# Performance work log

Measured on AMD Instinct MI355X. Metric: run time of the kernel, lower is better.

Reference implementation:

```python
import jax, jax.numpy as jnp
import numpy as np

E = 262144   # number of edges
B = 8192     # buckets per grouping
D = 32       # uniform bucket degree (B*D == E)
DIM = 128    # in_feats
OUT = 128    # out_feats


def setup_inputs() -> dict:
    key = jax.random.key(0)
    ks = jax.random.split(key, 12)
    src_feat = jax.random.normal(ks[0], (E, DIM), jnp.float32)
    dst_feat = jax.random.normal(ks[1], (E, DIM), jnp.float32)
    timestamp = jax.random.uniform(ks[2], (E,), jnp.float32) * 100.0
    # grouping permutations: flat edge order -> buckets of uniform degree
    src_perm = jax.random.permutation(ks[3], E).astype(jnp.int32)
    dst_perm = jax.random.permutation(ks[4], E).astype(jnp.int32)
    # causal deg_indices: index of most recent valid temporal neighbor, <= position
    pos = jnp.arange(D, dtype=jnp.int32)[None, :]
    src_deg_indices = jnp.minimum(jax.random.randint(ks[5], (B, D), 0, D, jnp.int32), pos)
    dst_deg_indices = jnp.minimum(jax.random.randint(ks[6], (B, D), 0, D, jnp.int32), pos)
    # TimeEncodingLayer('cosine') params
    basis_freq = 0.1 * jnp.linspace(0.0, 9.0, DIM, dtype=jnp.float32)
    phase = jnp.zeros((DIM,), jnp.float32)
    W_time = jax.random.normal(ks[7], (DIM, 2 * DIM), jnp.float32) * 0.05
    b_time = jnp.zeros((DIM,), jnp.float32)
    # fc_self / fc_neigh
    W_self = jax.random.normal(ks[8], (OUT, DIM), jnp.float32) * 0.05
    b_self = jnp.zeros((OUT,), jnp.float32)
    W_neigh = jax.random.normal(ks[9], (OUT, DIM), jnp.float32) * 0.05
    b_neigh = jnp.zeros((OUT,), jnp.float32)
    return dict(src_feat=src_feat, dst_feat=dst_feat, timestamp=timestamp,
                basis_freq=basis_freq, phase=phase, W_time=W_time, b_time=b_time,
                W_self=W_self, b_self=b_self, W_neigh=W_neigh, b_neigh=b_neigh,
                src_perm=src_perm, dst_perm=dst_perm,
                src_deg_indices=src_deg_indices, dst_deg_indices=dst_deg_indices)


def _encode_time(u, t, basis_freq, phase, W_time, b_time):
    # cosine time encoding: cos(t * freq + phase), concat with u, linear, relu
    tt = jnp.cos(t[:, None] * basis_freq[None, :] + phase[None, :])  # [E, DIM]
    x = jnp.concatenate([u, tt], axis=-1) @ W_time.T + b_time
    return jax.nn.relu(x)


def _mean_conv(h_self_e, h_neigh_e, perm, idx, W_self, b_self, W_neigh, b_neigh):
    # gather flat edge features into [B, D, DIM] buckets
    hs = h_self_e[perm].reshape(B, D, DIM)
    hn = h_neigh_e[perm].reshape(B, D, DIM)
    # mean aggregator: cumsum / (deg_indices+1), then gather at deg_indices
    mean_cof = (idx.astype(hn.dtype) + 1.0)[:, :, None]          # [B, D, 1]
    h_feat = jnp.cumsum(hn, axis=1) / mean_cof                    # [B, D, DIM]
    mask_feat = jnp.take_along_axis(h_feat, idx[:, :, None], axis=1)  # [B, D, DIM]
    rst = hs @ W_self.T + b_self + mask_feat @ W_neigh.T + b_neigh    # [B, D, OUT]
    # scatter back to flat edge order
    return jnp.zeros((E, OUT), rst.dtype).at[perm].set(rst.reshape(E, OUT))


def reference(src_feat, dst_feat, timestamp, basis_freq, phase, W_time, b_time,
              W_self, b_self, W_neigh, b_neigh,
              src_perm, dst_perm, src_deg_indices, dst_deg_indices):
    enc_src = _encode_time(src_feat, timestamp, basis_freq, phase, W_time, b_time)
    enc_dst = _encode_time(dst_feat, timestamp, basis_freq, phase, W_time, b_time)
    # groupby='src': self = src embedding, neighbors = dst embeddings
    src_out = _mean_conv(enc_src, enc_dst, src_perm, src_deg_indices,
                         W_self, b_self, W_neigh, b_neigh)
    # groupby='dst': self = dst embedding, neighbors = src embeddings
    dst_out = _mean_conv(enc_dst, enc_src, dst_perm, dst_deg_indices,
                         W_self, b_self, W_neigh, b_neigh)
    return src_out, dst_out
```

## Files before the change

kernel.cpp:

```cpp
#include <hip/hip_runtime.h>
#include <hip/hip_bf16.h>
#include <math.h>

#define E_EDGES 262144
#define NBUCKET 8192
#define DEG     32
#define FDIM    128

typedef float f32x4 __attribute__((ext_vector_type(4)));
typedef short s16x8 __attribute__((ext_vector_type(8)));
typedef short s16x4 __attribute__((ext_vector_type(4)));

typedef const __attribute__((address_space(1))) unsigned g_u32;
typedef __attribute__((address_space(3))) unsigned l_u32;

__device__ __forceinline__ short f2bf(float f) {
    __hip_bfloat16 h = __float2bfloat16(f);
    return *reinterpret_cast<short*>(&h);
}
__device__ __forceinline__ float bf2f(short s) {
    union { unsigned u; float f; } v; v.u = ((unsigned)(unsigned short)s) << 16;
    return v.f;
}

__device__ __forceinline__ s16x8 read_wfrag(const short* w_lds, int n, int k0) {
    int byte = ((n << 8) + (k0 << 1)) ^ ((n & 7) << 4);
    return *reinterpret_cast<const s16x8*>(reinterpret_cast<const char*>(w_lds) + byte);
}

__device__ __forceinline__ void stage_w(short* w_lds, const float* __restrict__ Wg,
                                        int stride, int tid) {
    #pragma unroll
    for (int it = 0; it < 16; ++it) {
        int i  = it * 256 + tid;
        int n  = i >> 5;
        int k4 = (i & 31) << 2;
        const float4 v = *reinterpret_cast<const float4*>(Wg + (size_t)n * stride + k4);
        s16x4 h; h[0]=f2bf(v.x); h[1]=f2bf(v.y); h[2]=f2bf(v.z); h[3]=f2bf(v.w);
        int byte = ((n << 8) + (k4 << 1)) ^ ((n & 7) << 4);
        *reinterpret_cast<s16x4*>(reinterpret_cast<char*>(w_lds) + byte) = h;
    }
}

__device__ __forceinline__ void dma_w32k(const short* __restrict__ gsw, short* lds, int tid) {
    const int lane = tid & 63, wid = tid >> 6;
    const char* g = reinterpret_cast<const char*>(gsw);
    char* l = reinterpret_cast<char*>(lds);
    #pragma unroll
    for (int i = 0; i < 8; ++i) {
        const int off = i * 4096 + wid * 1024;
        __builtin_amdgcn_global_load_lds((g_u32*)(g + off + lane * 16),
                                         (l_u32*)(l + off), 16, 0, 0);
    }
}

__global__ void prep_kernel(const float* __restrict__ W_time,
                            const float* __restrict__ W_self,
                            const float* __restrict__ W_neigh,
                            short* __restrict__ Wswz)
{
    const int t = blockIdx.x * 256 + threadIdx.x;
    const int region = t >> 11;
    const int chunk  = t & 2047;
    const int n = chunk >> 4;
    const int c = chunk & 15;

    const float* src;
    if      (region == 0) src = W_time  + n * 256 + c * 8;
    else if (region == 1) src = W_time  + n * 256 + 128 + c * 8;
    else if (region == 2) src = W_self  + n * 128 + c * 8;
    else                  src = W_neigh + n * 128 + c * 8;

    const float4 lo = *reinterpret_cast<const float4*>(src);
    const float4 hi = *reinterpret_cast<const float4*>(src + 4);
    s16x8 h;
    h[0]=f2bf(lo.x); h[1]=f2bf(lo.y); h[2]=f2bf(lo.z); h[3]=f2bf(lo.w);
    h[4]=f2bf(hi.x); h[5]=f2bf(hi.y); h[6]=f2bf(hi.z); h[7]=f2bf(hi.w);

    const int byte = (region << 15) + ((((n << 8) + (c << 4)) ^ ((n & 7) << 4)));
    *reinterpret_cast<s16x8*>(reinterpret_cast<char*>(Wswz) + byte) = h;
}

__global__ __launch_bounds__(512, 4)
void encode_kernel(const float* __restrict__ src_feat,
                   const float* __restrict__ dst_feat,
                   const float* __restrict__ ts,
                   const float* __restrict__ freq,
                   const float* __restrict__ ph,
                   const short* __restrict__ Wswz,
                   const float* __restrict__ b_time,
                   short* __restrict__ enc_src,
                   short* __restrict__ enc_dst)
{
    __shared__ short w_lds[2][128 * 128];

    const int tid  = threadIdx.x;
    const int lane = tid & 63;
    const int wid  = tid >> 6;
    const int lrow = lane & 15;
    const int q    = lane >> 4;
    const int klo  = q << 3;
    const int r0   = blockIdx.x * 128 + wid * 16;

    float4 sf[8], df[8];
    #pragma unroll
    for (int kb = 0; kb < 4; ++kb) {
        const float* ps = src_feat + (size_t)(r0 + lrow) * FDIM + kb * 32 + klo;
        const float* pd = dst_feat + (size_t)(r0 + lrow) * FDIM + kb * 32 + klo;
        sf[kb*2]   = *reinterpret_cast<const float4*>(ps);
        sf[kb*2+1] = *reinterpret_cast<const float4*>(ps + 4);
        df[kb*2]   = *reinterpret_cast<const float4*>(pd);
        df[kb*2+1] = *reinterpret_cast<const float4*>(pd + 4);
    }

    {
        const char* g = reinterpret_cast<const char*>(Wswz);
        char* l = reinterpret_cast<char*>(&w_lds[0][0]);
        #pragma unroll
        for (int i = 0; i < 8; ++i) {
            const int off = i * 8192 + wid * 1024;
            __builtin_amdgcn_global_load_lds((g_u32*)(g + off + lane * 16),
                                             (l_u32*)(l + off), 16, 0, 0);
        }
    }

    const float t_row = ts[r0 + lrow];
    s16x8 tf[4];
    #pragma unroll
    for (int kb = 0; kb < 4; ++kb) {
        s16x8 t;
        #pragma unroll
        for (int j = 0; j < 8; ++j) {
            const int k = kb * 32 + klo + j;
            t[j] = f2bf(__cosf(fmaf(t_row, freq[k], ph[k])));
        }
        tf[kb] = t;
    }

    s16x8 as_[4], ad_[4];
    #pragma unroll
    for (int kb = 0; kb < 4; ++kb) {
        s16x8 a, b;
        #pragma unroll
        for (int j = 0; j < 4; ++j) {
            a[j]   = f2bf(sf[kb*2][j]);   a[4+j] = f2bf(sf[kb*2+1][j]);
            b[j]   = f2bf(df[kb*2][j]);   b[4+j] = f2bf(df[kb*2+1][j]);
        }
        as_[kb] = a; ad_[kb] = b;
    }
    __syncthreads();

    #pragma unroll
    for (int nt = 0; nt < 8; ++nt) {
        const int n = nt * 16 + lrow;
        f32x4 a = {0.f, 0.f, 0.f, 0.f};
        #pragma unroll
        for (int kb = 0; kb < 4; ++kb)
            a = __builtin_amdgcn_mfma_f32_16x16x32_bf16(
                    read_wfrag(w_lds[1], n, kb * 32 + klo), tf[kb], a, 0, 0, 0);
        f32x4 b = a;
        #pragma unroll
        for (int kb = 0; kb < 4; ++kb) {
            const s16x8 wf = read_wfrag(w_lds[0], n, kb * 32 + klo);
            a = __builtin_amdgcn_mfma_f32_16x16x32_bf16(wf, as_[kb], a, 0, 0, 0);
            b = __builtin_amdgcn_mfma_f32_16x16x32_bf16(wf, ad_[kb], b, 0, 0, 0);
        }
        const int ch = nt * 16 + q * 4;
        const float4 bias4 = *reinterpret_cast<const float4*>(b_time + ch);
        s16x4 ss, sd;
        #pragma unroll
        for (int r = 0; r < 4; ++r) {
            float es = a[r] + bias4[r]; es = es > 0.f ? es : 0.f;
            float ed = b[r] + bias4[r]; ed = ed > 0.f ? ed : 0.f;
            ss[r] = f2bf(es); sd[r] = f2bf(ed);
        }
        *reinterpret_cast<s16x4*>(enc_src + (size_t)(r0 + lrow) * FDIM + ch) = ss;
        *reinterpret_cast<s16x4*>(enc_dst + (size_t)(r0 + lrow) * FDIM + ch) = sd;
    }
}

__global__ __launch_bounds__(256, 2)
void encode_fallback(const float* __restrict__ src_feat,
                     const float* __restrict__ dst_feat,
                     const float* __restrict__ ts,
                     const float* __restrict__ freq,
                     const float* __restrict__ ph,
                     const float* __restrict__ W_time,
                     const float* __restrict__ b_time,
                     short* __restrict__ enc_src,
                     short* __restrict__ enc_dst)
{
    __shared__ short w_lds[128 * 128];
    const int tid  = threadIdx.x;
    const int lane = tid & 63;
    const int wid  = tid >> 6;
    const int r0   = blockIdx.x * 64 + wid * 16;
    const int lrow = lane & 15;
    const int klo  = (lane >> 4) << 3;

    stage_w(w_lds, W_time + 128, 256, tid);
    const float t_row = ts[r0 + lrow];
    s16x8 tf[4];
    #pragma unroll
    for (int kb = 0; kb < 4; ++kb) {
        const int k = kb * 32 + klo;
        s16x8 t;
        #pragma unroll
        for (int j = 0; j < 8; ++j)
            t[j] = f2bf(__cosf(fmaf(t_row, freq[k + j], ph[k + j])));
        tf[kb] = t;
    }
    __syncthreads();
    f32x4 S[8];
    #pragma unroll
    for (int nt = 0; nt < 8; ++nt) {
        f32x4 a = {0.f, 0.f, 0.f, 0.f};
        #pragma unroll
        for (int kb = 0; kb < 4; ++kb)
            a = __builtin_amdgcn_mfma_f32_16x16x32_bf16(
                    tf[kb], read_wfrag(w_lds, nt * 16 + lrow, kb * 32 + klo), a, 0, 0, 0);
        S[nt] = a;
    }
    __syncthreads();
    stage_w(w_lds, W_time, 256, tid);
    __syncthreads();
    #pragma unroll
    for (int s = 0; s < 2; ++s) {
        const float* feat = s ? dst_feat : src_feat;
        short*       enc  = s ? enc_dst  : enc_src;
        s16x8 af[4];
        #pragma unroll
        for (int kb = 0; kb < 4; ++kb) {
            const float* p = feat + (size_t)(r0 + lrow) * FDIM + kb * 32 + klo;
            const float4 lo = *reinterpret_cast<const float4*>(p);
            const float4 hi = *reinterpret_cast<const float4*>(p + 4);
            s16x8 a;
            a[0]=f2bf(lo.x); a[1]=f2bf(lo.y); a[2]=f2bf(lo.z); a[3]=f2bf(lo.w);
            a[4]=f2bf(hi.x); a[5]=f2bf(hi.y); a[6]=f2bf(hi.z); a[7]=f2bf(hi.w);
            af[kb] = a;
        }
        #pragma unroll
        for (int nt = 0; nt < 8; ++nt) {
            f32x4 acc = S[nt];
            #pragma unroll
            for (int kb = 0; kb < 4; ++kb)
                acc = __builtin_amdgcn_mfma_f32_16x16x32_bf16(
                        af[kb], read_wfrag(w_lds, nt * 16 + lrow, kb * 32 + klo), acc, 0, 0, 0);
            const int col  = nt * 16 + lrow;
            const float bias = b_time[col];
            const int rbase = r0 + ((lane >> 4) << 2);
            #pragma unroll
            for (int r = 0; r < 4; ++r) {
                float e = acc[r] + bias;
                e = e > 0.f ? e : 0.f;
                enc[(size_t)(rbase + r) * FDIM + col] = f2bf(e);
            }
        }
    }
}

template<int DMA>
__global__ __launch_bounds__(256, 3)
void conv_kernel(const short* __restrict__ enc_src,
                 const short* __restrict__ enc_dst,
                 const short* __restrict__ Wswz_self,
                 const short* __restrict__ Wswz_neigh,
                 const float* __restrict__ W_self,
                 const float* __restrict__ W_neigh,
                 const float* __restrict__ b_self,
                 const float* __restrict__ b_neigh,
                 const int* __restrict__ src_perm,
                 const int* __restrict__ dst_perm,
                 const int* __restrict__ src_idx,
                 const int* __restrict__ dst_idx,
                 float* __restrict__ out)
{
    __shared__ short w_lds[128 * 128];
    __shared__ short hf[2][DEG * 128];
    __shared__ int   perm_s[2][DEG];
    __shared__ int   idx_s[2][DEG];
    __shared__ float bias_s[128];

    const int tid = threadIdx.x;
    const int g   = blockIdx.y;
    const int b0  = blockIdx.x * 2;

    const short* enc_self  = g ? enc_dst : enc_src;
    const short* enc_neigh = g ? enc_src : enc_dst;
    const int*   perm      = g ? dst_perm : src_perm;
    const int*   degi      = g ? dst_idx  : src_idx;
    float*       outg      = out + (size_t)g * E_EDGES * FDIM;

    if (DMA) dma_w32k(Wswz_self, w_lds, tid);

    if (tid < 64) {
        const int lb = tid >> 5, d = tid & 31;
        perm_s[lb][d] = perm[(b0 + lb) * DEG + d];
        idx_s[lb][d]  = degi[(b0 + lb) * DEG + d];
    } else if (tid < 192) {
        const int c = tid - 64;
        bias_s[c] = b_self[c] + b_neigh[c];
    }
    if (!DMA) stage_w(w_lds, W_self, 128, tid);
    __syncthreads();

    const int lane = tid & 63;
    const int wid  = tid >> 6;
    const int lb   = wid >> 1;
    const int mt   = wid & 1;
    const int lrow = lane & 15;
    const int klo  = (lane >> 4) << 3;
    const int row  = mt * 16 + lrow;

    s16x8 hsf[4];
    {
        const int e = perm_s[lb][row];
        const short* p = enc_self + (size_t)e * FDIM;
        #pragma unroll
        for (int kb = 0; kb < 4; ++kb)
            hsf[kb] = *reinterpret_cast<const s16x8*>(p + kb * 32 + klo);
    }

    const int lbc = tid >> 7;
    const int c   = tid & 127;
    unsigned short cum[DEG];
    #pragma unroll
    for (int d = 0; d < DEG; ++d) {
        const int e = perm_s[lbc][d];
        cum[d] = *reinterpret_cast<const unsigned short*>(
                     enc_neigh + (size_t)e * FDIM + c);
    }

    f32x4 acc[8];
    #pragma unroll
    for (int nt = 0; nt < 8; ++nt) {
        f32x4 a = {0.f, 0.f, 0.f, 0.f};
        #pragma unroll
        for (int kb = 0; kb < 4; ++kb)
            a = __builtin_amdgcn_mfma_f32_16x16x32_bf16(
                    hsf[kb], read_wfrag(w_lds, nt * 16 + lrow, kb * 32 + klo), a, 0, 0, 0);
        acc[nt] = a;
    }

    {
        float run = 0.f;
        #pragma unroll
        for (int d = 0; d < DEG; ++d) {
            run += bf2f((short)cum[d]);
            const float inv = __builtin_amdgcn_rcpf((float)(idx_s[lbc][d] + 1));
            const int byte = ((d << 8) + (c << 1)) ^ ((d & 7) << 4);
            *reinterpret_cast<short*>(reinterpret_cast<char*>(hf[lbc]) + byte)
                = f2bf(run * inv);
        }
    }

    __syncthreads();
    if (DMA) dma_w32k(Wswz_neigh, w_lds, tid);
    else     stage_w(w_lds, W_neigh, 128, tid);
    __syncthreads();

    s16x8 mff[4];
    {
        const int j = idx_s[lb][row];
        #pragma unroll
        for (int kb = 0; kb < 4; ++kb) {
            const int byte = ((j << 8) + ((kb * 32 + klo) << 1)) ^ ((j & 7) << 4);
            mff[kb] = *reinterpret_cast<const s16x8*>(
                          reinterpret_cast<const char*>(hf[lb]) + byte);
        }
    }
    #pragma unroll
    for (int nt = 0; nt < 8; ++nt) {
        f32x4 a = acc[nt];
        #pragma unroll
        for (int kb = 0; kb < 4; ++kb)
            a = __builtin_amdgcn_mfma_f32_16x16x32_bf16(
                    mff[kb], read_wfrag(w_lds, nt * 16 + lrow, kb * 32 + klo), a, 0, 0, 0);
        acc[nt] = a;
    }

    __syncthreads();
    {
        float* epl = reinterpret_cast<float*>(w_lds) + wid * 2048;
        #pragma unroll
        for (int nt = 0; nt < 8; ++nt) {
            const int col = nt * 16 + lrow;
            const float bias = bias_s[col];
            #pragma unroll
            for (int r = 0; r < 4; ++r) {
                const int rtile = ((lane >> 4) << 2) + r;
                epl[rtile * 128 + col] = acc[nt][r] + bias;
            }
        }
        asm volatile("s_waitcnt lgkmcnt(0)" ::: "memory");
        __builtin_amdgcn_sched_barrier(0);
        #pragma unroll
        for (int i = 0; i < 8; ++i) {
            const int rtile = i * 2 + (lane >> 5);
            const int c4    = (lane & 31) * 4;
            const f32x4 v = *reinterpret_cast<const f32x4*>(epl + rtile * 128 + c4);
            const int e = perm_s[lb][mt * 16 + rtile];
            *reinterpret_cast<f32x4*>(outg + (size_t)e * FDIM + c4) = v;
        }
    }
}

extern "C" void kernel_launch(void* const* d_in, const int* in_sizes, int n_in,
                              void* d_out, int out_size, void* d_ws, size_t ws_size,
                              hipStream_t stream) {
    (void)in_sizes; (void)n_in; (void)out_size;

    const float* src_feat = (const float*)d_in[0];
    const float* dst_feat = (const float*)d_in[1];
    const float* ts       = (const float*)d_in[2];
    const float* freq     = (const float*)d_in[3];
    const float* ph       = (const float*)d_in[4];
    const float* W_time   = (const float*)d_in[5];
    const float* b_time   = (const float*)d_in[6];
    const float* W_self   = (const float*)d_in[7];
    const float* b_self   = (const float*)d_in[8];
    const float* W_neigh  = (const float*)d_in[9];
    const float* b_neigh  = (const float*)d_in[10];
    const int*   src_perm = (const int*)d_in[11];
    const int*   dst_perm = (const int*)d_in[12];
    const int*   src_idx  = (const int*)d_in[13];
    const int*   dst_idx  = (const int*)d_in[14];

    short* enc_src = (short*)d_ws;
    short* enc_dst = enc_src + (size_t)E_EDGES * FDIM;
    short* Wswz    = enc_dst + (size_t)E_EDGES * FDIM;
    const size_t need = (size_t)E_EDGES * FDIM * 2 * 2 + 4 * 32768;

    if (ws_size >= need) {
        prep_kernel<<<dim3(32), dim3(256), 0, stream>>>(W_time, W_self, W_neigh, Wswz);
        encode_kernel<<<dim3(E_EDGES / 128), dim3(512), 0, stream>>>(
            src_feat, dst_feat, ts, freq, ph, Wswz, b_time, enc_src, enc_dst);
        conv_kernel<1><<<dim3(NBUCKET / 2, 2), dim3(256), 0, stream>>>(
            enc_src, enc_dst, Wswz + 2 * 16384, Wswz + 3 * 16384, W_self, W_neigh,
            b_self, b_neigh, src_perm, dst_perm, src_idx, dst_idx, (float*)d_out);
    } else {
        encode_fallback<<<dim3(E_EDGES / 64), dim3(256), 0, stream>>>(
            src_feat, dst_feat, ts, freq, ph, W_time, b_time, enc_src, enc_dst);
        conv_kernel<0><<<dim3(NBUCKET / 2, 2), dim3(256), 0, stream>>>(
            enc_src, enc_dst, (const short*)nullptr, (const short*)nullptr,
            W_self, W_neigh, b_self, b_neigh,
            src_perm, dst_perm, src_idx, dst_idx, (float*)d_out);
    }
}
```

Baseline: 241.1 us.

## Make encode kernel persistent over 4 row tiles with register prefetch

Each encode block now handles four 128-row tiles instead of one, so the 64KB time-weight load into LDS is paid once per four tiles. The next tile's source and destination features and timestamp are loaded into registers while the current tile's MFMAs run, overlapping global loads with compute. In exchange the grid shrinks fourfold (512 blocks) and register pressure rises, which can lower occupancy and latency hiding.

```diff
diff --git a/kernel.cpp b/kernel.cpp
--- a/kernel.cpp
+++ b/kernel.cpp
@@ -6,6 +6,7 @@
 #define NBUCKET 8192
 #define DEG     32
 #define FDIM    128
+#define ENC_TILES 4
 
 typedef float f32x4 __attribute__((ext_vector_type(4)));
 typedef short s16x8 __attribute__((ext_vector_type(8)));
@@ -100,18 +101,7 @@
     const int lrow = lane & 15;
     const int q    = lane >> 4;
     const int klo  = q << 3;
-    const int r0   = blockIdx.x * 128 + wid * 16;
-
-    float4 sf[8], df[8];
-    #pragma unroll
-    for (int kb = 0; kb < 4; ++kb) {
-        const float* ps = src_feat + (size_t)(r0 + lrow) * FDIM + kb * 32 + klo;
-        const float* pd = dst_feat + (size_t)(r0 + lrow) * FDIM + kb * 32 + klo;
-        sf[kb*2]   = *reinterpret_cast<const float4*>(ps);
-        sf[kb*2+1] = *reinterpret_cast<const float4*>(ps + 4);
-        df[kb*2]   = *reinterpret_cast<const float4*>(pd);
-        df[kb*2+1] = *reinterpret_cast<const float4*>(pd + 4);
-    }
+    const int base = blockIdx.x * (128 * ENC_TILES) + wid * 16 + lrow;
 
     {
         const char* g = reinterpret_cast<const char*>(Wswz);
@@ -124,58 +114,93 @@
         }
     }
 
-    const float t_row = ts[r0 + lrow];
-    s16x8 tf[4];
-    #pragma unroll
-    for (int kb = 0; kb < 4; ++kb) {
-        s16x8 t;
-        #pragma unroll
-        for (int j = 0; j < 8; ++j) {
-            const int k = kb * 32 + klo + j;
-            t[j] = f2bf(__cosf(fmaf(t_row, freq[k], ph[k])));
-        }
-        tf[kb] = t;
-    }
-
-    s16x8 as_[4], ad_[4];
-    #pragma unroll
-    for (int kb = 0; kb < 4; ++kb) {
-        s16x8 a, b;
-        #pragma unroll
-        for (int j = 0; j < 4; ++j) {
-            a[j]   = f2bf(sf[kb*2][j]);   a[4+j] = f2bf(sf[kb*2+1][j]);
-            b[j]   = f2bf(df[kb*2][j]);   b[4+j] = f2bf(df[kb*2+1][j]);
-        }
-        as_[kb] = a; ad_[kb] = b;
-    }
-    __syncthreads();
-
-    #pragma unroll
-    for (int nt = 0; nt < 8; ++nt) {
-        const int n = nt * 16 + lrow;
-        f32x4 a = {0.f, 0.f, 0.f, 0.f};
-        #pragma unroll
-        for (int kb = 0; kb < 4; ++kb)
-            a = __builtin_amdgcn_mfma_f32_16x16x32_bf16(
-                    read_wfrag(w_lds[1], n, kb * 32 + klo), tf[kb], a, 0, 0, 0);
-        f32x4 b = a;
+    float4 sf[8], df[8];
+    {
+        const float* ps = src_feat + (size_t)base * FDIM + klo;
+        const float* pd = dst_feat + (size_t)base * FDIM + klo;
         #pragma unroll
         for (int kb = 0; kb < 4; ++kb) {
-            const s16x8 wf = read_wfrag(w_lds[0], n, kb * 32 + klo);
-            a = __builtin_amdgcn_mfma_f32_16x16x32_bf16(wf, as_[kb], a, 0, 0, 0);
-            b = __builtin_amdgcn_mfma_f32_16x16x32_bf16(wf, ad_[kb], b, 0, 0, 0);
-        }
-        const int ch = nt * 16 + q * 4;
-        const float4 bias4 = *reinterpret_cast<const float4*>(b_time + ch);
-        s16x4 ss, sd;
-        #pragma unroll
-        for (int r = 0; r < 4; ++r) {
-            float es = a[r] + bias4[r]; es = es > 0.f ? es : 0.f;
-            float ed = b[r] + bias4[r]; ed = ed > 0.f ? ed : 0.f;
-            ss[r] = f2bf(es); sd[r] = f2bf(ed);
-        }
-        *reinterpret_cast<s16x4*>(enc_src + (size_t)(r0 + lrow) * FDIM + ch) = ss;
-        *reinterpret_cast<s16x4*>(enc_dst + (size_t)(r0 + lrow) * FDIM + ch) = sd;
+            sf[kb*2]   = *reinterpret_cast<const float4*>(ps + kb * 32);
+            sf[kb*2+1] = *reinterpret_cast<const float4*>(ps + kb * 32 + 4);
+            df[kb*2]   = *reinterpret_cast<const float4*>(pd + kb * 32);
+            df[kb*2+1] = *reinterpret_cast<const float4*>(pd + kb * 32 + 4);
+        }
+    }
+    float t_cur = ts[base];
+
+    __syncthreads();
+
+    for (int it = 0; it < ENC_TILES; ++it) {
+        const int r = base + it * 128;
+
+        s16x8 as_[4], ad_[4];
+        #pragma unroll
+        for (int kb = 0; kb < 4; ++kb) {
+            s16x8 a, b;
+            #pragma unroll
+            for (int j = 0; j < 4; ++j) {
+                a[j]   = f2bf(sf[kb*2][j]);   a[4+j] = f2bf(sf[kb*2+1][j]);
+                b[j]   = f2bf(df[kb*2][j]);   b[4+j] = f2bf(df[kb*2+1][j]);
+            }
+            as_[kb] = a; ad_[kb] = b;
+        }
+
+        float t_next = 0.f;
+        if (it + 1 < ENC_TILES) {
+            const int rn = r + 128;
+            const float* ps = src_feat + (size_t)rn * FDIM + klo;
+            const float* pd = dst_feat + (size_t)rn * FDIM + klo;
+            #pragma unroll
+            for (int kb = 0; kb < 4; ++kb) {
+                sf[kb*2]   = *reinterpret_cast<const float4*>(ps + kb * 32);
+                sf[kb*2+1] = *reinterpret_cast<const float4*>(ps + kb * 32 + 4);
+                df[kb*2]   = *reinterpret_cast<const float4*>(pd + kb * 32);
+                df[kb*2+1] = *reinterpret_cast<const float4*>(pd + kb * 32 + 4);
+            }
+            t_next = ts[rn];
+        }
+
+        s16x8 tf[4];
+        #pragma unroll
+        for (int kb = 0; kb < 4; ++kb) {
+            s16x8 t;
+            #pragma unroll
+            for (int j = 0; j < 8; ++j) {
+                const int k = kb * 32 + klo + j;
+                t[j] = f2bf(__cosf(fmaf(t_cur, freq[k], ph[k])));
+            }
+            tf[kb] = t;
+        }
+
+        #pragma unroll
+        for (int nt = 0; nt < 8; ++nt) {
+            const int n = nt * 16 + lrow;
+            f32x4 a = {0.f, 0.f, 0.f, 0.f};
+            #pragma unroll
+            for (int kb = 0; kb < 4; ++kb)
+                a = __builtin_amdgcn_mfma_f32_16x16x32_bf16(
+                        read_wfrag(w_lds[1], n, kb * 32 + klo), tf[kb], a, 0, 0, 0);
+            f32x4 b = a;
+            #pragma unroll
+            for (int kb = 0; kb < 4; ++kb) {
+                const s16x8 wf = read_wfrag(w_lds[0], n, kb * 32 + klo);
+                a = __builtin_amdgcn_mfma_f32_16x16x32_bf16(wf, as_[kb], a, 0, 0, 0);
+                b = __builtin_amdgcn_mfma_f32_16x16x32_bf16(wf, ad_[kb], b, 0, 0, 0);
+            }
+            const int ch = nt * 16 + q * 4;
+            const float4 bias4 = *reinterpret_cast<const float4*>(b_time + ch);
+            s16x4 ss, sd;
+            #pragma unroll
+            for (int rr = 0; rr < 4; ++rr) {
+                float es = a[rr] + bias4[rr]; es = es > 0.f ? es : 0.f;
+                float ed = b[rr] + bias4[rr]; ed = ed > 0.f ? ed : 0.f;
+                ss[rr] = f2bf(es); sd[rr] = f2bf(ed);
+            }
+            *reinterpret_cast<s16x4*>(enc_src + (size_t)r * FDIM + ch) = ss;
+            *reinterpret_cast<s16x4*>(enc_dst + (size_t)r * FDIM + ch) = sd;
+        }
+
+        t_cur = t_next;
     }
 }
 
@@ -433,7 +458,7 @@
 
     if (ws_size >= need) {
         prep_kernel<<<dim3(32), dim3(256), 0, stream>>>(W_time, W_self, W_neigh, Wswz);
-        encode_kernel<<<dim3(E_EDGES / 128), dim3(512), 0, stream>>>(
+        encode_kernel<<<dim3(E_EDGES / (128 * ENC_TILES)), dim3(512), 0, stream>>>(
             src_feat, dst_feat, ts, freq, ph, Wswz, b_time, enc_src, enc_dst);
         conv_kernel<1><<<dim3(NBUCKET / 2, 2), dim3(256), 0, stream>>>(
             enc_src, enc_dst, Wswz + 2 * 16384, Wswz + 3 * 16384, W_self, W_neigh,
```

Result: slower. 820.2 us (+240.2%).
